# Performance work log

Hardware: AMD Instinct MI355X
Metric: run time of the kernel (lower is better)

The kernel has to match this reference:

```python
import jax, jax.numpy as jnp
import numpy as np
from jax import lax

D_MODEL = 1024
EXPAND = 2
D_INNER = EXPAND * D_MODEL        # 2048
D_STATE = 16
D_CONV = 4
DT_RANK = (D_MODEL + 15) // 16    # 64, standard 'auto' dt_rank
BATCH, SEQ = 2, 1024


def setup_inputs() -> dict:
    key = jax.random.key(0)
    ks = jax.random.split(key, 10)
    g = lambda k, shape, sc: jax.random.normal(k, shape, jnp.float32) * sc
    A_log = jnp.log(jnp.broadcast_to(
        jnp.arange(1, D_STATE + 1, dtype=jnp.float32), (D_INNER, D_STATE)))
    return {
        "x": jax.random.normal(ks[0], (BATCH, SEQ, D_MODEL), jnp.float32),
        "gamma": jnp.ones((D_MODEL,), jnp.float32),
        "beta": jnp.zeros((D_MODEL,), jnp.float32),
        "W_in": g(ks[1], (D_MODEL, 2 * D_INNER), 0.02),
        "W_conv": g(ks[2], (D_INNER, D_CONV), 0.1),
        "b_conv": jnp.zeros((D_INNER,), jnp.float32),
        "W_x": g(ks[3], (D_INNER, DT_RANK + 2 * D_STATE), 0.02),
        "W_dt": g(ks[4], (DT_RANK, D_INNER), 0.1),
        "b_dt": g(ks[5], (D_INNER,), 0.1),
        "A_log": A_log,
        "Dskip": jnp.ones((D_INNER,), jnp.float32),
        "W_out": g(ks[6], (D_INNER, D_MODEL), 0.02),
    }


def _layernorm(x, gamma, beta, eps=1e-5):
    mu = jnp.mean(x, axis=-1, keepdims=True)
    var = jnp.mean(jnp.square(x - mu), axis=-1, keepdims=True)
    return (x - mu) * lax.rsqrt(var + eps) * gamma + beta


def _mamba_block(x, gamma, beta, W_in, W_conv, b_conv, W_x, W_dt, b_dt,
                 A_log, Dskip, W_out):
    h = _layernorm(x, gamma, beta)                       # [B,L,D]
    xz = h @ W_in                                        # [B,L,2*Din]
    xi, z = jnp.split(xz, 2, axis=-1)                    # each [B,L,Din]

    # depthwise causal conv over time
    xt = xi.transpose(0, 2, 1)                           # [B,Din,L]
    conv = lax.conv_general_dilated(
        xt, W_conv[:, None, :], window_strides=(1,),
        padding=[(D_CONV - 1, 0)], feature_group_count=D_INNER)
    u = jax.nn.silu(conv + b_conv[None, :, None]).transpose(0, 2, 1)  # [B,L,Din]

    x_dbl = u @ W_x                                      # [B,L,dt_rank+2N]
    dt_r = x_dbl[..., :DT_RANK]
    Bm = x_dbl[..., DT_RANK:DT_RANK + D_STATE]           # [B,L,N]
    Cm = x_dbl[..., DT_RANK + D_STATE:]                  # [B,L,N]
    dt = jax.nn.softplus(dt_r @ W_dt + b_dt)             # [B,L,Din]

    A = -jnp.exp(A_log)                                  # [Din,N]

    def step(hstate, inp):
        dt_s, B_s, C_s, u_s = inp                        # [B,Din],[B,N],[B,N],[B,Din]
        dA = jnp.exp(dt_s[..., None] * A)                # [B,Din,N]
        hstate = dA * hstate + (dt_s * u_s)[..., None] * B_s[:, None, :]
        y = jnp.einsum('bdn,bn->bd', hstate, C_s)
        return hstate, y

    h0 = jnp.zeros((x.shape[0], D_INNER, D_STATE), x.dtype)
    _, ys = lax.scan(step, h0, (dt.transpose(1, 0, 2), Bm.transpose(1, 0, 2),
                                Cm.transpose(1, 0, 2), u.transpose(1, 0, 2)))
    y = ys.transpose(1, 0, 2) + u * Dskip                # [B,L,Din]
    y = y * jax.nn.silu(z)
    return x + y @ W_out                                 # residual


def reference(x, gamma, beta, W_in, W_conv, b_conv, W_x, W_dt, b_dt,
              A_log, Dskip, W_out):
    return _mamba_block(x, gamma, beta, W_in, W_conv, b_conv, W_x, W_dt,
                        b_dt, A_log, Dskip, W_out)
```

## Files before the change

kernel.cpp:

```cpp
#include <hip/hip_runtime.h>
#include <math.h>

#define BB 2
#define SS 1024
#define DM 1024
#define DI 2048
#define DSTATE 16
#define DTR 64
#define NX 96
#define ROWS (BB*SS)
#define NCHUNK 16
#define LC (SS/NCHUNK)
#define NCH (BB*DI)
#define TS 16
#define NT (LC/TS)
#define KSPLIT 4
#define KSX 16

typedef __bf16 bf16x8 __attribute__((ext_vector_type(8)));
typedef float f32x4 __attribute__((ext_vector_type(4)));

static __device__ __forceinline__ unsigned short f2bf(float f) {
    unsigned u = __builtin_bit_cast(unsigned, f);
    unsigned r = (u + 0x7fff + ((u >> 16) & 1)) >> 16;
    return (unsigned short)r;
}

__device__ __forceinline__ void transpose_body(const float* __restrict__ W,
                                               unsigned short* __restrict__ WT,
                                               int K, int N, int bx, int by,
                                               unsigned short (*tile)[33]) {
    int n0 = bx * 32, k0 = by * 32;
    int tx = threadIdx.x & 31, ty = threadIdx.x >> 5;
#pragma unroll
    for (int r = 0; r < 4; r++)
        tile[ty + r * 8][tx] = f2bf(W[(size_t)(k0 + ty + r * 8) * N + n0 + tx]);
    __syncthreads();
#pragma unroll
    for (int r = 0; r < 4; r++)
        WT[(size_t)(n0 + ty + r * 8) * K + k0 + tx] = tile[tx][ty + r * 8];
}

__global__ __launch_bounds__(256) void prep_kernel(const float* __restrict__ x,
                                                   const float* __restrict__ gamma,
                                                   const float* __restrict__ beta,
                                                   unsigned short* __restrict__ h,
                                                   const float* __restrict__ W_in,
                                                   unsigned short* __restrict__ W_inT,
                                                   const float* __restrict__ W_out,
                                                   unsigned short* __restrict__ W_outT,
                                                   const float* __restrict__ W_x,
                                                   unsigned short* __restrict__ W_xT,
                                                   const float* __restrict__ W_dt,
                                                   unsigned short* __restrict__ W_dtT) {
    __shared__ unsigned short tile[32][33];
    __shared__ float red[4], red2[4];
    int blk = blockIdx.x;
    if (blk < ROWS) {
        int row = blk;
        const float* xr = x + (size_t)row * DM;
        float v[4];
        float s = 0.f;
#pragma unroll
        for (int i = 0; i < 4; i++) { v[i] = xr[threadIdx.x + i * 256]; s += v[i]; }
        int lane = threadIdx.x & 63, wid = threadIdx.x >> 6;
#pragma unroll
        for (int m = 1; m < 64; m <<= 1) s += __shfl_xor(s, m);
        if (lane == 0) red[wid] = s;
        __syncthreads();
        float mean = (red[0] + red[1] + red[2] + red[3]) * (1.0f / DM);
        float vs = 0.f;
#pragma unroll
        for (int i = 0; i < 4; i++) { float dv = v[i] - mean; vs += dv * dv; }
#pragma unroll
        for (int m = 1; m < 64; m <<= 1) vs += __shfl_xor(vs, m);
        if (lane == 0) red2[wid] = vs;
        __syncthreads();
        float var = (red2[0] + red2[1] + red2[2] + red2[3]) * (1.0f / DM);
        float inv = rsqrtf(var + 1e-5f);
        unsigned short* hr = h + (size_t)row * DM;
#pragma unroll
        for (int i = 0; i < 4; i++) {
            int idx = threadIdx.x + i * 256;
            hr[idx] = f2bf((v[i] - mean) * inv * gamma[idx] + beta[idx]);
        }
        return;
    }
    blk -= ROWS;
    if (blk < 4096) { transpose_body(W_in, W_inT, DM, 2 * DI, blk % 128, blk / 128, tile); return; }
    blk -= 4096;
    if (blk < 2048) { transpose_body(W_out, W_outT, DI, DM, blk % 32, blk / 32, tile); return; }
    blk -= 2048;
    if (blk < 192) { transpose_body(W_x, W_xT, DI, NX, blk % 3, blk / 3, tile); return; }
    blk -= 192;
    transpose_body(W_dt, W_dtT, DTR, DI, blk % 64, blk / 64, tile);
}

__global__ __launch_bounds__(256) void gemm_mfma_bfout(const __bf16* __restrict__ A,
                                                       const __bf16* __restrict__ BT,
                                                       unsigned short* __restrict__ C,
                                                       int M, int N, int K) {
    __shared__ __bf16 As[128 * 32];
    __shared__ __bf16 Bs[128 * 32];
    int tid = threadIdx.x;
    int w = tid >> 6, lane = tid & 63;
    int wr = w >> 1, wc = w & 1;
    int m0 = blockIdx.y * 128, n0 = blockIdx.x * 128;
    f32x4 acc[4][4] = {};
    int srow = lane >> 2, sgran = lane & 3;
    const __bf16* gA = A + (size_t)(m0 + w * 32) * K;
    const __bf16* gB = BT + (size_t)(n0 + w * 32) * K;
    int fr = lane & 15, q = lane >> 4;

    for (int k0 = 0; k0 < K; k0 += 32) {
        __syncthreads();
#pragma unroll
        for (int c = 0; c < 2; c++) {
            const __bf16* ga = gA + (size_t)(c * 16 + srow) * K + k0 + sgran * 8;
            const __bf16* gb = gB + (size_t)(c * 16 + srow) * K + k0 + sgran * 8;
            __builtin_amdgcn_global_load_lds(
                (const __attribute__((address_space(1))) void*)ga,
                (__attribute__((address_space(3))) void*)&As[(w * 32 + c * 16) * 32], 16, 0, 0);
            __builtin_amdgcn_global_load_lds(
                (const __attribute__((address_space(1))) void*)gb,
                (__attribute__((address_space(3))) void*)&Bs[(w * 32 + c * 16) * 32], 16, 0, 0);
        }
        __syncthreads();
        bf16x8 af[4], bfr[4];
#pragma unroll
        for (int i = 0; i < 4; i++)
            af[i] = *(const bf16x8*)&As[(wr * 64 + i * 16 + fr) * 32 + q * 8];
#pragma unroll
        for (int j = 0; j < 4; j++)
            bfr[j] = *(const bf16x8*)&Bs[(wc * 64 + j * 16 + fr) * 32 + q * 8];
#pragma unroll
        for (int i = 0; i < 4; i++)
#pragma unroll
            for (int j = 0; j < 4; j++)
                acc[i][j] = __builtin_amdgcn_mfma_f32_16x16x32_bf16(af[i], bfr[j], acc[i][j], 0, 0, 0);
    }
#pragma unroll
    for (int i = 0; i < 4; i++)
#pragma unroll
        for (int j = 0; j < 4; j++)
#pragma unroll
            for (int r = 0; r < 4; r++) {
                size_t ro = (size_t)(m0 + wr * 64 + i * 16 + q * 4 + r) * N
                          + n0 + wc * 64 + j * 16 + fr;
                C[ro] = f2bf(acc[i][j][r]);
            }
}

__global__ __launch_bounds__(256) void gemm_mfma_splitk(const __bf16* __restrict__ A,
                                                        const __bf16* __restrict__ BT,
                                                        float* __restrict__ part,
                                                        int M, int N, int K) {
    __shared__ __bf16 As[128 * 32];
    __shared__ __bf16 Bs[128 * 32];
    int tid = threadIdx.x;
    int w = tid >> 6, lane = tid & 63;
    int wr = w >> 1, wc = w & 1;
    int m0 = blockIdx.y * 128, n0 = blockIdx.x * 128;
    int ks = K / KSPLIT;
    int kbase = blockIdx.z * ks;
    f32x4 acc[4][4] = {};
    int srow = lane >> 2, sgran = lane & 3;
    const __bf16* gA = A + (size_t)(m0 + w * 32) * K + kbase;
    const __bf16* gB = BT + (size_t)(n0 + w * 32) * K + kbase;
    int fr = lane & 15, q = lane >> 4;

    for (int k0 = 0; k0 < ks; k0 += 32) {
        __syncthreads();
#pragma unroll
        for (int c = 0; c < 2; c++) {
            const __bf16* ga = gA + (size_t)(c * 16 + srow) * K + k0 + sgran * 8;
            const __bf16* gb = gB + (size_t)(c * 16 + srow) * K + k0 + sgran * 8;
            __builtin_amdgcn_global_load_lds(
                (const __attribute__((address_space(1))) void*)ga,
                (__attribute__((address_space(3))) void*)&As[(w * 32 + c * 16) * 32], 16, 0, 0);
            __builtin_amdgcn_global_load_lds(
                (const __attribute__((address_space(1))) void*)gb,
                (__attribute__((address_space(3))) void*)&Bs[(w * 32 + c * 16) * 32], 16, 0, 0);
        }
        __syncthreads();
        bf16x8 af[4], bfr[4];
#pragma unroll
        for (int i = 0; i < 4; i++)
            af[i] = *(const bf16x8*)&As[(wr * 64 + i * 16 + fr) * 32 + q * 8];
#pragma unroll
        for (int j = 0; j < 4; j++)
            bfr[j] = *(const bf16x8*)&Bs[(wc * 64 + j * 16 + fr) * 32 + q * 8];
#pragma unroll
        for (int i = 0; i < 4; i++)
#pragma unroll
            for (int j = 0; j < 4; j++)
                acc[i][j] = __builtin_amdgcn_mfma_f32_16x16x32_bf16(af[i], bfr[j], acc[i][j], 0, 0, 0);
    }
    float* Cp = part + (size_t)blockIdx.z * M * N;
#pragma unroll
    for (int i = 0; i < 4; i++)
#pragma unroll
        for (int j = 0; j < 4; j++)
#pragma unroll
            for (int r = 0; r < 4; r++) {
                size_t ro = (size_t)(m0 + wr * 64 + i * 16 + q * 4 + r) * N
                          + n0 + wc * 64 + j * 16 + fr;
                Cp[ro] = acc[i][j][r];
            }
}

__global__ __launch_bounds__(256) void reduce_splitk(const float* __restrict__ part,
                                                     const float* __restrict__ x,
                                                     float* __restrict__ out) {
    size_t i4 = ((size_t)blockIdx.x * 256 + threadIdx.x) * 4;
    const size_t slice = (size_t)ROWS * DM;
    f32x4 s = *(const f32x4*)(x + i4);
#pragma unroll
    for (int z = 0; z < KSPLIT; z++) {
        f32x4 p = *(const f32x4*)(part + z * slice + i4);
        s.x += p.x; s.y += p.y; s.z += p.z; s.w += p.w;
    }
    *(f32x4*)(out + i4) = s;
}

__global__ __launch_bounds__(256) void gemm_mfma_xdbl(const __bf16* __restrict__ A,
                                                      const __bf16* __restrict__ BT,
                                                      float* __restrict__ part_x) {
    __shared__ __bf16 As[128 * 32];
    __shared__ __bf16 Bs[128 * 32];
    int tid = threadIdx.x;
    int w = tid >> 6, lane = tid & 63;
    int wr = w >> 1, wc = w & 1;
    int m0 = blockIdx.y * 128;
    int srow = lane >> 2, sgran = lane & 3;
    int fr = lane & 15, q = lane >> 4;
    f32x4 acc[4][4] = {};
    const int ks = DI / KSX;
    const int kbase = blockIdx.z * ks;
    const __bf16* gA = A + (size_t)(m0 + w * 32) * DI + kbase;

    for (int k0 = 0; k0 < ks; k0 += 32) {
        __syncthreads();
#pragma unroll
        for (int c = 0; c < 2; c++) {
            const __bf16* ga = gA + (size_t)(c * 16 + srow) * DI + k0 + sgran * 8;
            int brow = w * 32 + c * 16 + srow;
            if (brow > 95) brow = 95;
            const __bf16* gb = BT + (size_t)brow * DI + kbase + k0 + sgran * 8;
            __builtin_amdgcn_global_load_lds(
                (const __attribute__((address_space(1))) void*)ga,
                (__attribute__((address_space(3))) void*)&As[(w * 32 + c * 16) * 32], 16, 0, 0);
            __builtin_amdgcn_global_load_lds(
                (const __attribute__((address_space(1))) void*)gb,
                (__attribute__((address_space(3))) void*)&Bs[(w * 32 + c * 16) * 32], 16, 0, 0);
        }
        __syncthreads();
        bf16x8 af[4], bfr[4];
#pragma unroll
        for (int i = 0; i < 4; i++)
            af[i] = *(const bf16x8*)&As[(wr * 64 + i * 16 + fr) * 32 + q * 8];
#pragma unroll
        for (int j = 0; j < 4; j++)
            bfr[j] = *(const bf16x8*)&Bs[(wc * 64 + j * 16 + fr) * 32 + q * 8];
#pragma unroll
        for (int i = 0; i < 4; i++)
#pragma unroll
            for (int j = 0; j < 4; j++)
                acc[i][j] = __builtin_amdgcn_mfma_f32_16x16x32_bf16(af[i], bfr[j], acc[i][j], 0, 0, 0);
    }
    float* Cp = part_x + (size_t)blockIdx.z * ROWS * NX;
#pragma unroll
    for (int i = 0; i < 4; i++)
#pragma unroll
        for (int j = 0; j < 4; j++) {
            int col = wc * 64 + j * 16 + fr;
            if (col < NX) {
#pragma unroll
                for (int r = 0; r < 4; r++) {
                    int row = m0 + wr * 64 + i * 16 + q * 4 + r;
                    Cp[(size_t)row * NX + col] = acc[i][j][r];
                }
            }
        }
}

__global__ __launch_bounds__(256) void reduce_xdbl(const float* __restrict__ part_x,
                                                   float* __restrict__ xdbl,
                                                   unsigned short* __restrict__ dtr_bf) {
    int idx = blockIdx.x * 256 + threadIdx.x;
    const size_t slice = (size_t)ROWS * NX;
    float s = 0.f;
#pragma unroll
    for (int z = 0; z < KSX; z++) s += part_x[z * slice + idx];
    xdbl[idx] = s;
    int col = idx % NX;
    if (col < DTR) {
        int row = idx / NX;
        dtr_bf[(size_t)row * DTR + col] = f2bf(s);
    }
}

__global__ __launch_bounds__(256) void dt_gemm(const __bf16* __restrict__ A,
                                               const __bf16* __restrict__ BT,
                                               const float* __restrict__ b_dt,
                                               unsigned short* __restrict__ dt) {
    __shared__ __bf16 As[128 * 32];
    __shared__ __bf16 Bs[128 * 32];
    int tid = threadIdx.x;
    int w = tid >> 6, lane = tid & 63;
    int wr = w >> 1, wc = w & 1;
    int m0 = blockIdx.y * 128, n0 = blockIdx.x * 128;
    int srow = lane >> 2, sgran = lane & 3;
    int fr = lane & 15, q = lane >> 4;
    f32x4 acc[4][4] = {};
    const __bf16* gA = A + (size_t)(m0 + w * 32) * DTR;
    const __bf16* gB = BT + (size_t)(n0 + w * 32) * DTR;

    for (int k0 = 0; k0 < DTR; k0 += 32) {
        __syncthreads();
#pragma unroll
        for (int c = 0; c < 2; c++) {
            const __bf16* ga = gA + (size_t)(c * 16 + srow) * DTR + k0 + sgran * 8;
            const __bf16* gb = gB + (size_t)(c * 16 + srow) * DTR + k0 + sgran * 8;
            __builtin_amdgcn_global_load_lds(
                (const __attribute__((address_space(1))) void*)ga,
                (__attribute__((address_space(3))) void*)&As[(w * 32 + c * 16) * 32], 16, 0, 0);
            __builtin_amdgcn_global_load_lds(
                (const __attribute__((address_space(1))) void*)gb,
                (__attribute__((address_space(3))) void*)&Bs[(w * 32 + c * 16) * 32], 16, 0, 0);
        }
        __syncthreads();
        bf16x8 af[4], bfr[4];
#pragma unroll
        for (int i = 0; i < 4; i++)
            af[i] = *(const bf16x8*)&As[(wr * 64 + i * 16 + fr) * 32 + q * 8];
#pragma unroll
        for (int j = 0; j < 4; j++)
            bfr[j] = *(const bf16x8*)&Bs[(wc * 64 + j * 16 + fr) * 32 + q * 8];
#pragma unroll
        for (int i = 0; i < 4; i++)
#pragma unroll
            for (int j = 0; j < 4; j++)
                acc[i][j] = __builtin_amdgcn_mfma_f32_16x16x32_bf16(af[i], bfr[j], acc[i][j], 0, 0, 0);
    }
#pragma unroll
    for (int i = 0; i < 4; i++)
#pragma unroll
        for (int j = 0; j < 4; j++) {
            int col = n0 + wc * 64 + j * 16 + fr;
            float bv = b_dt[col];
#pragma unroll
            for (int r = 0; r < 4; r++) {
                int row = m0 + wr * 64 + i * 16 + q * 4 + r;
                float a = acc[i][j][r] + bv;
                float sp = (a > 20.f) ? a : log1pf(expf(a));
                dt[(size_t)row * DI + col] = f2bf(sp);
            }
        }
}

__global__ __launch_bounds__(256) void conv_silu(const __bf16* __restrict__ xz,
                                                 const float* __restrict__ Wc,
                                                 const float* __restrict__ bc,
                                                 unsigned short* __restrict__ u_bf) {
    int idx = blockIdx.x * 256 + threadIdx.x;
    int d = idx & (DI - 1);
    int row = idx >> 11;
    int tpos = row & (SS - 1);
    float acc = bc[d];
#pragma unroll
    for (int k = 0; k < 4; k++) {
        int tt = tpos - 3 + k;
        if (tt >= 0) acc += (float)xz[(size_t)(row - 3 + k) * (2 * DI) + d] * Wc[d * 4 + k];
    }
    float s = acc / (1.f + __expf(-acc));
    u_bf[idx] = f2bf(s);
}

__global__ __launch_bounds__(256) void scan_chunk1(const __bf16* __restrict__ dt,
                                                   const __bf16* __restrict__ u,
                                                   const float* __restrict__ xdbl,
                                                   const float* __restrict__ A_log,
                                                   float* __restrict__ Aprod,
                                                   float* __restrict__ hloc) {
    __shared__ __bf16 dts[TS * 256];
    __shared__ __bf16 us_[TS * 256];
    __shared__ float bs[LC * DSTATE];
    int tid = threadIdx.x;
    int d0 = blockIdx.x * 256;
    int db = d0 & (DI - 1);
    int j = blockIdx.y;
    int c = d0 + tid;
    int b = c >> 11;
    int d = c & (DI - 1);
    int w = tid >> 6, lane = tid & 63;
    int halfrow = lane >> 5;
    int cw = (lane & 31) * 8;
    size_t r0 = (size_t)b * SS + (size_t)j * LC;

    {
        int row = tid >> 2, col = (tid & 3) * 4;
        f32x4 v = *(const f32x4*)(xdbl + (r0 + row) * NX + DTR + col);
        *(f32x4*)&bs[row * DSTATE + col] = v;
    }
    float Av[DSTATE], h[DSTATE], P[DSTATE];
#pragma unroll
    for (int q = 0; q < 4; q++) {
        f32x4 al = *(const f32x4*)(A_log + (size_t)d * DSTATE + q * 4);
#pragma unroll
        for (int e = 0; e < 4; e++) {
            Av[q * 4 + e] = -expf(al[e]);
            h[q * 4 + e] = 0.f;
            P[q * 4 + e] = 1.f;
        }
    }

    for (int tile = 0; tile < NT; tile++) {
        int t0 = tile * TS;
#pragma unroll
        for (int i = 0; i < 2; i++) {
            int rl = w * 4 + i * 2;
            const __bf16* gdt = dt + (size_t)(r0 + t0 + rl + halfrow) * DI + db + cw;
            const __bf16* gu  = u  + (size_t)(r0 + t0 + rl + halfrow) * DI + db + cw;
            __builtin_amdgcn_global_load_lds(
                (const __attribute__((address_space(1))) void*)gdt,
                (__attribute__((address_space(3))) void*)&dts[rl * 256], 16, 0, 0);
            __builtin_amdgcn_global_load_lds(
                (const __attribute__((address_space(1))) void*)gu,
                (__attribute__((address_space(3))) void*)&us_[rl * 256], 16, 0, 0);
        }
        __syncthreads();
#pragma unroll
        for (int t = 0; t < TS; t++) {
            float dtv = (float)dts[t * 256 + tid];
            float uv  = (float)us_[t * 256 + tid];
            float du = dtv * uv;
            const float* br = &bs[(t0 + t) * DSTATE];
            f32x4 Bq[4] = {*(const f32x4*)&br[0], *(const f32x4*)&br[4],
                           *(const f32x4*)&br[8], *(const f32x4*)&br[12]};
#pragma unroll
            for (int n = 0; n < DSTATE; n++) {
                float dA = __expf(dtv * Av[n]);
                P[n] *= dA;
                h[n] = dA * h[n] + du * Bq[n >> 2][n & 3];
            }
        }
        __syncthreads();
    }
    f32x4* Po = (f32x4*)(Aprod + ((size_t)j * NCH + c) * DSTATE);
    f32x4* ho = (f32x4*)(hloc + ((size_t)j * NCH + c) * DSTATE);
#pragma unroll
    for (int q = 0; q < 4; q++) {
        Po[q] = *(f32x4*)&P[q * 4];
        ho[q] = *(f32x4*)&h[q * 4];
    }
}

__global__ __launch_bounds__(256) void scan_chunk2(const __bf16* __restrict__ dt,
                                                   const __bf16* __restrict__ u,
                                                   const float* __restrict__ xdbl,
                                                   const float* __restrict__ A_log,
                                                   const float* __restrict__ Aprod,
                                                   const float* __restrict__ hloc,
                                                   const __bf16* __restrict__ xz,
                                                   const float* __restrict__ Dskip,
                                                   unsigned short* __restrict__ y2) {
    __shared__ __bf16 dts[TS * 256];
    __shared__ __bf16 us_[TS * 256];
    __shared__ __bf16 zs[TS * 256];
    __shared__ float bcs[LC * 2 * DSTATE];
    int tid = threadIdx.x;
    int d0 = blockIdx.x * 256;
    int db = d0 & (DI - 1);
    int j = blockIdx.y;
    int c = d0 + tid;
    int b = c >> 11;
    int d = c & (DI - 1);
    int w = tid >> 6, lane = tid & 63;
    int halfrow = lane >> 5;
    int cw = (lane & 31) * 8;
    size_t r0 = (size_t)b * SS + (size_t)j * LC;

    {
        int row = tid >> 2, col = (tid & 3) * 8;
        const float* src = xdbl + (r0 + row) * NX + DTR + col;
        f32x4 v0 = *(const f32x4*)src;
        f32x4 v1 = *(const f32x4*)(src + 4);
        *(f32x4*)&bcs[row * 32 + col] = v0;
        *(f32x4*)&bcs[row * 32 + col + 4] = v1;
    }
    float Av[DSTATE], h[DSTATE];
#pragma unroll
    for (int q = 0; q < 4; q++) {
        f32x4 al = *(const f32x4*)(A_log + (size_t)d * DSTATE + q * 4);
#pragma unroll
        for (int e = 0; e < 4; e++) {
            Av[q * 4 + e] = -expf(al[e]);
            h[q * 4 + e] = 0.f;
        }
    }
    for (int jj = 0; jj < j; jj++) {
        const f32x4* Pp = (const f32x4*)(Aprod + ((size_t)jj * NCH + c) * DSTATE);
        const f32x4* Hp = (const f32x4*)(hloc + ((size_t)jj * NCH + c) * DSTATE);
#pragma unroll
        for (int q = 0; q < 4; q++) {
            f32x4 P = Pp[q], H = Hp[q];
#pragma unroll
            for (int e = 0; e < 4; e++)
                h[q * 4 + e] = P[e] * h[q * 4 + e] + H[e];
        }
    }
    float Dv = Dskip[d];

    for (int tile = 0; tile < NT; tile++) {
        int t0 = tile * TS;
#pragma unroll
        for (int i = 0; i < 2; i++) {
            int rl = w * 4 + i * 2;
            const __bf16* gdt = dt + (size_t)(r0 + t0 + rl + halfrow) * DI + db + cw;
            const __bf16* gu  = u  + (size_t)(r0 + t0 + rl + halfrow) * DI + db + cw;
            const __bf16* gz  = xz + (size_t)(r0 + t0 + rl + halfrow) * (2 * DI) + DI + db + cw;
            __builtin_amdgcn_global_load_lds(
                (const __attribute__((address_space(1))) void*)gdt,
                (__attribute__((address_space(3))) void*)&dts[rl * 256], 16, 0, 0);
            __builtin_amdgcn_global_load_lds(
                (const __attribute__((address_space(1))) void*)gu,
                (__attribute__((address_space(3))) void*)&us_[rl * 256], 16, 0, 0);
            __builtin_amdgcn_global_load_lds(
                (const __attribute__((address_space(1))) void*)gz,
                (__attribute__((address_space(3))) void*)&zs[rl * 256], 16, 0, 0);
        }
        __syncthreads();
#pragma unroll
        for (int t = 0; t < TS; t++) {
            float dtv = (float)dts[t * 256 + tid];
            float uv  = (float)us_[t * 256 + tid];
            float zz  = (float)zs[t * 256 + tid];
            float du = dtv * uv;
            const float* br = &bcs[(t0 + t) * 32];
            f32x4 Bq[4] = {*(const f32x4*)&br[0], *(const f32x4*)&br[4],
                           *(const f32x4*)&br[8], *(const f32x4*)&br[12]};
            f32x4 Cq[4] = {*(const f32x4*)&br[16], *(const f32x4*)&br[20],
                           *(const f32x4*)&br[24], *(const f32x4*)&br[28]};
            float p = 0.f;
#pragma unroll
            for (int n = 0; n < DSTATE; n++) {
                float dA = __expf(dtv * Av[n]);
                h[n] = dA * h[n] + du * Bq[n >> 2][n & 3];
                p += h[n] * Cq[n >> 2][n & 3];
            }
            float sz = zz / (1.f + __expf(-zz));
            y2[(r0 + t0 + t) * DI + d] = f2bf((p + uv * Dv) * sz);
        }
        __syncthreads();
    }
}

extern "C" void kernel_launch(void* const* d_in, const int* in_sizes, int n_in,
                              void* d_out, int out_size, void* d_ws, size_t ws_size,
                              hipStream_t stream) {
    const float* x      = (const float*)d_in[0];
    const float* gamma  = (const float*)d_in[1];
    const float* beta   = (const float*)d_in[2];
    const float* W_in   = (const float*)d_in[3];
    const float* W_conv = (const float*)d_in[4];
    const float* b_conv = (const float*)d_in[5];
    const float* W_x    = (const float*)d_in[6];
    const float* W_dt   = (const float*)d_in[7];
    const float* b_dt   = (const float*)d_in[8];
    const float* A_log  = (const float*)d_in[9];
    const float* Dskip  = (const float*)d_in[10];
    const float* W_out  = (const float*)d_in[11];
    float* out = (float*)d_out;

    float* ws     = (float*)d_ws;
    float* xdbl   = ws;
    float* Aprod  = xdbl + (size_t)ROWS * NX;
    float* hloc   = Aprod + (size_t)NCHUNK * NCH * DSTATE;
    float* part   = hloc + (size_t)NCHUNK * NCH * DSTATE;
    float* part_x = part + (size_t)KSPLIT * ROWS * DM;
    unsigned short* xz_bf  = (unsigned short*)(part_x + (size_t)KSX * ROWS * NX);
    unsigned short* u_bf   = xz_bf + (size_t)ROWS * 2 * DI;
    unsigned short* dt_bf  = u_bf + (size_t)ROWS * DI;
    unsigned short* h_bf   = dt_bf + (size_t)ROWS * DI;
    unsigned short* y_bf   = h_bf + (size_t)ROWS * DM;
    unsigned short* W_inT  = y_bf + (size_t)ROWS * DI;
    unsigned short* W_outT = W_inT + (size_t)(2 * DI) * DM;
    unsigned short* W_xT   = W_outT + (size_t)DM * DI;
    unsigned short* W_dtT  = W_xT + (size_t)NX * DI;
    unsigned short* dtr_bf = W_dtT + (size_t)DI * DTR;

    prep_kernel<<<ROWS + 4096 + 2048 + 192 + 128, 256, 0, stream>>>(
        x, gamma, beta, h_bf, W_in, W_inT, W_out, W_outT, W_x, W_xT, W_dt, W_dtT);
    gemm_mfma_bfout<<<dim3(2 * DI / 128, ROWS / 128), 256, 0, stream>>>(
        (const __bf16*)h_bf, (const __bf16*)W_inT, xz_bf, ROWS, 2 * DI, DM);
    conv_silu<<<ROWS * DI / 256, 256, 0, stream>>>((const __bf16*)xz_bf, W_conv, b_conv, u_bf);
    gemm_mfma_xdbl<<<dim3(1, ROWS / 128, KSX), 256, 0, stream>>>(
        (const __bf16*)u_bf, (const __bf16*)W_xT, part_x);
    reduce_xdbl<<<(ROWS * NX) / 256, 256, 0, stream>>>(part_x, xdbl, dtr_bf);
    dt_gemm<<<dim3(DI / 128, ROWS / 128), 256, 0, stream>>>(
        (const __bf16*)dtr_bf, (const __bf16*)W_dtT, b_dt, dt_bf);
    scan_chunk1<<<dim3(NCH / 256, NCHUNK), 256, 0, stream>>>(
        (const __bf16*)dt_bf, (const __bf16*)u_bf, xdbl, A_log, Aprod, hloc);
    scan_chunk2<<<dim3(NCH / 256, NCHUNK), 256, 0, stream>>>(
        (const __bf16*)dt_bf, (const __bf16*)u_bf, xdbl, A_log, Aprod, hloc,
        (const __bf16*)xz_bf, Dskip, y_bf);
    gemm_mfma_splitk<<<dim3(DM / 128, ROWS / 128, KSPLIT), 256, 0, stream>>>(
        (const __bf16*)y_bf, (const __bf16*)W_outT, part, ROWS, DM, DI);
    reduce_splitk<<<(ROWS * DM) / (256 * 4), 256, 0, stream>>>(part, x, out);
}
```

Baseline: 275.3 us.

## Fuse two-pass chunked scan into one cooperative kernel with grid sync

Merges scan_chunk1 and scan_chunk2 into a single cooperative kernel. Each block loads its whole chunk of dt, u and z into LDS once, runs the local scan, writes the chunk's decay product and state, then waits on a grid-wide barrier before combining prefix states and producing outputs from the data already in LDS. This removes one kernel launch and the second global read of dt and u. In exchange LDS use per block grows to roughly 100KB, which limits occupancy and requires all 256 blocks to be co-resident for the grid sync.

```diff
diff --git a/kernel.cpp b/kernel.cpp
--- a/kernel.cpp
+++ b/kernel.cpp
@@ -1,4 +1,5 @@
 #include <hip/hip_runtime.h>
+#include <hip/hip_cooperative_groups.h>
 #include <math.h>
 
 #define BB 2
@@ -12,8 +13,6 @@
 #define NCHUNK 16
 #define LC (SS/NCHUNK)
 #define NCH (BB*DI)
-#define TS 16
-#define NT (LC/TS)
 #define KSPLIT 4
 #define KSX 16
 
@@ -377,97 +376,18 @@
     u_bf[idx] = f2bf(s);
 }
 
-__global__ __launch_bounds__(256) void scan_chunk1(const __bf16* __restrict__ dt,
-                                                   const __bf16* __restrict__ u,
-                                                   const float* __restrict__ xdbl,
-                                                   const float* __restrict__ A_log,
-                                                   float* __restrict__ Aprod,
-                                                   float* __restrict__ hloc) {
-    __shared__ __bf16 dts[TS * 256];
-    __shared__ __bf16 us_[TS * 256];
-    __shared__ float bs[LC * DSTATE];
-    int tid = threadIdx.x;
-    int d0 = blockIdx.x * 256;
-    int db = d0 & (DI - 1);
-    int j = blockIdx.y;
-    int c = d0 + tid;
-    int b = c >> 11;
-    int d = c & (DI - 1);
-    int w = tid >> 6, lane = tid & 63;
-    int halfrow = lane >> 5;
-    int cw = (lane & 31) * 8;
-    size_t r0 = (size_t)b * SS + (size_t)j * LC;
-
-    {
-        int row = tid >> 2, col = (tid & 3) * 4;
-        f32x4 v = *(const f32x4*)(xdbl + (r0 + row) * NX + DTR + col);
-        *(f32x4*)&bs[row * DSTATE + col] = v;
-    }
-    float Av[DSTATE], h[DSTATE], P[DSTATE];
-#pragma unroll
-    for (int q = 0; q < 4; q++) {
-        f32x4 al = *(const f32x4*)(A_log + (size_t)d * DSTATE + q * 4);
-#pragma unroll
-        for (int e = 0; e < 4; e++) {
-            Av[q * 4 + e] = -expf(al[e]);
-            h[q * 4 + e] = 0.f;
-            P[q * 4 + e] = 1.f;
-        }
-    }
-
-    for (int tile = 0; tile < NT; tile++) {
-        int t0 = tile * TS;
-#pragma unroll
-        for (int i = 0; i < 2; i++) {
-            int rl = w * 4 + i * 2;
-            const __bf16* gdt = dt + (size_t)(r0 + t0 + rl + halfrow) * DI + db + cw;
-            const __bf16* gu  = u  + (size_t)(r0 + t0 + rl + halfrow) * DI + db + cw;
-            __builtin_amdgcn_global_load_lds(
-                (const __attribute__((address_space(1))) void*)gdt,
-                (__attribute__((address_space(3))) void*)&dts[rl * 256], 16, 0, 0);
-            __builtin_amdgcn_global_load_lds(
-                (const __attribute__((address_space(1))) void*)gu,
-                (__attribute__((address_space(3))) void*)&us_[rl * 256], 16, 0, 0);
-        }
-        __syncthreads();
-#pragma unroll
-        for (int t = 0; t < TS; t++) {
-            float dtv = (float)dts[t * 256 + tid];
-            float uv  = (float)us_[t * 256 + tid];
-            float du = dtv * uv;
-            const float* br = &bs[(t0 + t) * DSTATE];
-            f32x4 Bq[4] = {*(const f32x4*)&br[0], *(const f32x4*)&br[4],
-                           *(const f32x4*)&br[8], *(const f32x4*)&br[12]};
-#pragma unroll
-            for (int n = 0; n < DSTATE; n++) {
-                float dA = __expf(dtv * Av[n]);
-                P[n] *= dA;
-                h[n] = dA * h[n] + du * Bq[n >> 2][n & 3];
-            }
-        }
-        __syncthreads();
-    }
-    f32x4* Po = (f32x4*)(Aprod + ((size_t)j * NCH + c) * DSTATE);
-    f32x4* ho = (f32x4*)(hloc + ((size_t)j * NCH + c) * DSTATE);
-#pragma unroll
-    for (int q = 0; q < 4; q++) {
-        Po[q] = *(f32x4*)&P[q * 4];
-        ho[q] = *(f32x4*)&h[q * 4];
-    }
-}
-
-__global__ __launch_bounds__(256) void scan_chunk2(const __bf16* __restrict__ dt,
-                                                   const __bf16* __restrict__ u,
-                                                   const float* __restrict__ xdbl,
-                                                   const float* __restrict__ A_log,
-                                                   const float* __restrict__ Aprod,
-                                                   const float* __restrict__ hloc,
-                                                   const __bf16* __restrict__ xz,
-                                                   const float* __restrict__ Dskip,
-                                                   unsigned short* __restrict__ y2) {
-    __shared__ __bf16 dts[TS * 256];
-    __shared__ __bf16 us_[TS * 256];
-    __shared__ __bf16 zs[TS * 256];
+__global__ __launch_bounds__(256) void scan_fused(const __bf16* __restrict__ dt,
+                                                  const __bf16* __restrict__ u,
+                                                  const float* __restrict__ xdbl,
+                                                  const float* __restrict__ A_log,
+                                                  float* __restrict__ Aprod,
+                                                  float* __restrict__ hloc,
+                                                  const __bf16* __restrict__ xz,
+                                                  const float* __restrict__ Dskip,
+                                                  unsigned short* __restrict__ y2) {
+    __shared__ __bf16 dts[LC * 256];
+    __shared__ __bf16 us_[LC * 256];
+    __shared__ __bf16 zs[LC * 256];
     __shared__ float bcs[LC * 2 * DSTATE];
     int tid = threadIdx.x;
     int d0 = blockIdx.x * 256;
@@ -481,6 +401,22 @@
     int cw = (lane & 31) * 8;
     size_t r0 = (size_t)b * SS + (size_t)j * LC;
 
+#pragma unroll
+    for (int i = 0; i < 8; i++) {
+        int rl = w * 16 + i * 2;
+        const __bf16* gdt = dt + (size_t)(r0 + rl + halfrow) * DI + db + cw;
+        const __bf16* gu  = u  + (size_t)(r0 + rl + halfrow) * DI + db + cw;
+        const __bf16* gz  = xz + (size_t)(r0 + rl + halfrow) * (2 * DI) + DI + db + cw;
+        __builtin_amdgcn_global_load_lds(
+            (const __attribute__((address_space(1))) void*)gdt,
+            (__attribute__((address_space(3))) void*)&dts[rl * 256], 16, 0, 0);
+        __builtin_amdgcn_global_load_lds(
+            (const __attribute__((address_space(1))) void*)gu,
+            (__attribute__((address_space(3))) void*)&us_[rl * 256], 16, 0, 0);
+        __builtin_amdgcn_global_load_lds(
+            (const __attribute__((address_space(1))) void*)gz,
+            (__attribute__((address_space(3))) void*)&zs[rl * 256], 16, 0, 0);
+    }
     {
         int row = tid >> 2, col = (tid & 3) * 8;
         const float* src = xdbl + (r0 + row) * NX + DTR + col;
@@ -489,7 +425,7 @@
         *(f32x4*)&bcs[row * 32 + col] = v0;
         *(f32x4*)&bcs[row * 32 + col + 4] = v1;
     }
-    float Av[DSTATE], h[DSTATE];
+    float Av[DSTATE], h[DSTATE], P[DSTATE];
 #pragma unroll
     for (int q = 0; q < 4; q++) {
         f32x4 al = *(const f32x4*)(A_log + (size_t)d * DSTATE + q * 4);
@@ -497,62 +433,71 @@
         for (int e = 0; e < 4; e++) {
             Av[q * 4 + e] = -expf(al[e]);
             h[q * 4 + e] = 0.f;
-        }
-    }
+            P[q * 4 + e] = 1.f;
+        }
+    }
+    __syncthreads();
+
+    for (int t = 0; t < LC; t++) {
+        float dtv = (float)dts[t * 256 + tid];
+        float uv  = (float)us_[t * 256 + tid];
+        float du = dtv * uv;
+        const float* br = &bcs[t * 32];
+        f32x4 Bq[4] = {*(const f32x4*)&br[0], *(const f32x4*)&br[4],
+                       *(const f32x4*)&br[8], *(const f32x4*)&br[12]};
+#pragma unroll
+        for (int n = 0; n < DSTATE; n++) {
+            float dA = __expf(dtv * Av[n]);
+            P[n] *= dA;
+            h[n] = dA * h[n] + du * Bq[n >> 2][n & 3];
+        }
+    }
+    if (j < NCHUNK - 1) {
+        f32x4* Po = (f32x4*)(Aprod + ((size_t)j * NCH + c) * DSTATE);
+        f32x4* ho = (f32x4*)(hloc + ((size_t)j * NCH + c) * DSTATE);
+#pragma unroll
+        for (int q = 0; q < 4; q++) {
+            Po[q] = *(f32x4*)&P[q * 4];
+            ho[q] = *(f32x4*)&h[q * 4];
+        }
+    }
+    __threadfence();
+    cooperative_groups::this_grid().sync();
+
+#pragma unroll
+    for (int n = 0; n < DSTATE; n++) h[n] = 0.f;
     for (int jj = 0; jj < j; jj++) {
         const f32x4* Pp = (const f32x4*)(Aprod + ((size_t)jj * NCH + c) * DSTATE);
         const f32x4* Hp = (const f32x4*)(hloc + ((size_t)jj * NCH + c) * DSTATE);
 #pragma unroll
         for (int q = 0; q < 4; q++) {
-            f32x4 P = Pp[q], H = Hp[q];
+            f32x4 Pv = Pp[q], Hv = Hp[q];
 #pragma unroll
             for (int e = 0; e < 4; e++)
-                h[q * 4 + e] = P[e] * h[q * 4 + e] + H[e];
+                h[q * 4 + e] = Pv[e] * h[q * 4 + e] + Hv[e];
         }
     }
     float Dv = Dskip[d];
 
-    for (int tile = 0; tile < NT; tile++) {
-        int t0 = tile * TS;
-#pragma unroll
-        for (int i = 0; i < 2; i++) {
-            int rl = w * 4 + i * 2;
-            const __bf16* gdt = dt + (size_t)(r0 + t0 + rl + halfrow) * DI + db + cw;
-            const __bf16* gu  = u  + (size_t)(r0 + t0 + rl + halfrow) * DI + db + cw;
-            const __bf16* gz  = xz + (size_t)(r0 + t0 + rl + halfrow) * (2 * DI) + DI + db + cw;
-            __builtin_amdgcn_global_load_lds(
-                (const __attribute__((address_space(1))) void*)gdt,
-                (__attribute__((address_space(3))) void*)&dts[rl * 256], 16, 0, 0);
-            __builtin_amdgcn_global_load_lds(
-                (const __attribute__((address_space(1))) void*)gu,
-                (__attribute__((address_space(3))) void*)&us_[rl * 256], 16, 0, 0);
-            __builtin_amdgcn_global_load_lds(
-                (const __attribute__((address_space(1))) void*)gz,
-                (__attribute__((address_space(3))) void*)&zs[rl * 256], 16, 0, 0);
-        }
-        __syncthreads();
-#pragma unroll
-        for (int t = 0; t < TS; t++) {
-            float dtv = (float)dts[t * 256 + tid];
-            float uv  = (float)us_[t * 256 + tid];
-            float zz  = (float)zs[t * 256 + tid];
-            float du = dtv * uv;
-            const float* br = &bcs[(t0 + t) * 32];
-            f32x4 Bq[4] = {*(const f32x4*)&br[0], *(const f32x4*)&br[4],
-                           *(const f32x4*)&br[8], *(const f32x4*)&br[12]};
-            f32x4 Cq[4] = {*(const f32x4*)&br[16], *(const f32x4*)&br[20],
-                           *(const f32x4*)&br[24], *(const f32x4*)&br[28]};
-            float p = 0.f;
-#pragma unroll
-            for (int n = 0; n < DSTATE; n++) {
-                float dA = __expf(dtv * Av[n]);
-                h[n] = dA * h[n] + du * Bq[n >> 2][n & 3];
-                p += h[n] * Cq[n >> 2][n & 3];
-            }
-            float sz = zz / (1.f + __expf(-zz));
-            y2[(r0 + t0 + t) * DI + d] = f2bf((p + uv * Dv) * sz);
-        }
-        __syncthreads();
+    for (int t = 0; t < LC; t++) {
+        float dtv = (float)dts[t * 256 + tid];
+        float uv  = (float)us_[t * 256 + tid];
+        float zz  = (float)zs[t * 256 + tid];
+        float du = dtv * uv;
+        const float* br = &bcs[t * 32];
+        f32x4 Bq[4] = {*(const f32x4*)&br[0], *(const f32x4*)&br[4],
+                       *(const f32x4*)&br[8], *(const f32x4*)&br[12]};
+        f32x4 Cq[4] = {*(const f32x4*)&br[16], *(const f32x4*)&br[20],
+                       *(const f32x4*)&br[24], *(const f32x4*)&br[28]};
+        float p = 0.f;
+#pragma unroll
+        for (int n = 0; n < DSTATE; n++) {
+            float dA = __expf(dtv * Av[n]);
+            h[n] = dA * h[n] + du * Bq[n >> 2][n & 3];
+            p += h[n] * Cq[n >> 2][n & 3];
+        }
+        float sz = zz / (1.f + __expf(-zz));
+        y2[(r0 + t) * DI + d] = f2bf((p + uv * Dv) * sz);
     }
 }
 
@@ -600,11 +545,20 @@
     reduce_xdbl<<<(ROWS * NX) / 256, 256, 0, stream>>>(part_x, xdbl, dtr_bf);
     dt_gemm<<<dim3(DI / 128, ROWS / 128), 256, 0, stream>>>(
         (const __bf16*)dtr_bf, (const __bf16*)W_dtT, b_dt, dt_bf);
-    scan_chunk1<<<dim3(NCH / 256, NCHUNK), 256, 0, stream>>>(
-        (const __bf16*)dt_bf, (const __bf16*)u_bf, xdbl, A_log, Aprod, hloc);
-    scan_chunk2<<<dim3(NCH / 256, NCHUNK), 256, 0, stream>>>(
-        (const __bf16*)dt_bf, (const __bf16*)u_bf, xdbl, A_log, Aprod, hloc,
-        (const __bf16*)xz_bf, Dskip, y_bf);
+    {
+        const __bf16* a0 = (const __bf16*)dt_bf;
+        const __bf16* a1 = (const __bf16*)u_bf;
+        const float* a2 = xdbl;
+        const float* a3 = A_log;
+        float* a4 = Aprod;
+        float* a5 = hloc;
+        const __bf16* a6 = (const __bf16*)xz_bf;
+        const float* a7 = Dskip;
+        unsigned short* a8 = y_bf;
+        void* args[] = {&a0, &a1, &a2, &a3, &a4, &a5, &a6, &a7, &a8};
+        hipLaunchCooperativeKernel((void*)scan_fused, dim3(NCH / 256, NCHUNK),
+                                   dim3(256), args, 0, stream);
+    }
     gemm_mfma_splitk<<<dim3(DM / 128, ROWS / 128, KSPLIT), 256, 0, stream>>>(
         (const __bf16*)y_bf, (const __bf16*)W_outT, part, ROWS, DM, DI);
     reduce_splitk<<<(ROWS * DM) / (256 * 4), 256, 0, stream>>>(part, x, out);
```

Result: slower. 374.8 us (+36.1%).
